# Optimization experiments

Hardware: AMD Instinct MI355X
Metric: run time of the kernel (lower is better)

Reference implementation:

```python
import jax, jax.numpy as jnp
import numpy as np

B, S, E, H = 8, 512, 1024, 16
D = E // H  # head_dim = 64


def _rope_tables(seq_len, head_dim):
    inv_freq = 1.0 / (10000.0 ** (np.arange(0, head_dim, 2, dtype=np.float32) / head_dim))
    pos = np.arange(seq_len, dtype=np.float32)
    ang = np.einsum('i,j->ij', pos, inv_freq)  # [S, D/2]
    return jnp.asarray(np.cos(ang)), jnp.asarray(np.sin(ang))


def setup_inputs() -> dict:
    key = jax.random.key(0)
    ks = jax.random.split(key, 12)
    std = 1.0 / np.sqrt(E)
    inp = {
        'x_q': jax.random.normal(ks[0], (B, S, E), jnp.float32),
        'x_k': jax.random.normal(ks[1], (B, S, E), jnp.float32),
        'x_v': jax.random.normal(ks[2], (B, S, E), jnp.float32),
        'Wq': jax.random.normal(ks[3], (E, E), jnp.float32) * std,
        'bq': jnp.zeros((E,), jnp.float32),
        'Wk': jax.random.normal(ks[4], (E, E), jnp.float32) * std,
        'bk': jnp.zeros((E,), jnp.float32),
        'Wv': jax.random.normal(ks[5], (E, E), jnp.float32) * std,
        'bv': jnp.zeros((E,), jnp.float32),
        'Wo': jax.random.normal(ks[6], (E, E), jnp.float32) * std,
        'bo': jnp.zeros((E,), jnp.float32),
        'temperature': jnp.ones((), jnp.float32),
    }
    cos, sin = _rope_tables(S, D)
    inp['cos'] = cos
    inp['sin'] = sin
    return inp


def reference(x_q, x_k, x_v, Wq, bq, Wk, bk, Wv, bv, Wo, bo, temperature, cos, sin):
    b, s, e = x_q.shape
    h, d = H, D

    def proj(x, W, bias):
        # torch Linear: x @ W.T + b ; then split heads -> [b, h, s, d]
        y = jnp.einsum('bse,fe->bsf', x, W) + bias
        return y.reshape(b, s, h, d).transpose(0, 2, 1, 3)

    q = proj(x_q, Wq, bq)
    k = proj(x_k, Wk, bk)
    v = proj(x_v, Wv, bv)

    c = cos[:s]  # [s, d/2]
    sn = sin[:s]

    def rope(t):
        # interleaved pairing: view as [..., d/2, 2]
        t2 = t.reshape(b, h, s, d // 2, 2)
        t0, t1 = t2[..., 0], t2[..., 1]
        r = jnp.stack([t0 * c - t1 * sn, t0 * sn + t1 * c], axis=-1)
        return r.reshape(b, h, s, d)

    q = rope(q)
    k = rope(k)

    def l2norm(t):
        # torch F.normalize: x / max(||x||, eps)
        n = jnp.sqrt(jnp.sum(t * t, axis=-1, keepdims=True))
        return t / jnp.maximum(n, 1e-12)

    q = l2norm(q)
    k = l2norm(k)

    scores = jnp.einsum('bhqd,bhkd->bhqk', q, k) * temperature
    attn = jax.nn.softmax(scores, axis=-1)
    out = jnp.einsum('bhqk,bhkd->bhqd', attn, v)
    out = out.transpose(0, 2, 1, 3).reshape(b, s, e)
    return jnp.einsum('bse,fe->bsf', out, Wo) + bo
```

## Files before the change

### kernel.cpp

```cpp
#include <hip/hip_runtime.h>
#include <stdint.h>

#define DEV __device__ __forceinline__

typedef __bf16 bf16x8 __attribute__((ext_vector_type(8)));
typedef float f32x4 __attribute__((ext_vector_type(4)));
typedef unsigned short u16;
typedef u16 u16x8 __attribute__((ext_vector_type(8)));
typedef u16 u16x4 __attribute__((ext_vector_type(4)));
typedef __attribute__((address_space(3))) uint8_t lds8;
typedef __attribute__((address_space(1))) const uint8_t glb8;

constexpr int Bb = 8, Ss = 512, Ee = 1024, Hh = 16;
constexpr int BS = Bb * Ss;

DEV u16 f2bf(float f) {
  union { float f; uint32_t u; } v; v.f = f;
  return (u16)((v.u + 0x7FFFu + ((v.u >> 16) & 1u)) >> 16);
}
DEV bf16x8 ldsbf8(const u16* p) {
  u16x8 u = *(const u16x8*)p;
  return __builtin_bit_cast(bf16x8, u);
}
DEV f32x4 mfma16(bf16x8 a, bf16x8 b, f32x4 c) {
  return __builtin_amdgcn_mfma_f32_16x16x32_bf16(a, b, c, 0, 0, 0);
}

struct ConvArgs {
  const float* s[7];
  u16* d[7];
  int n[7];
};

__global__ __launch_bounds__(256) void convert_k(ConvArgs a) {
  int z = blockIdx.y;
  int base = (blockIdx.x * 256 + threadIdx.x) * 8;
  if (base >= a.n[z]) return;
  const float4* sp = (const float4*)(a.s[z] + base);
  float4 v0 = sp[0], v1 = sp[1];
  u16x8 o;
  o[0] = f2bf(v0.x); o[1] = f2bf(v0.y); o[2] = f2bf(v0.z); o[3] = f2bf(v0.w);
  o[4] = f2bf(v1.x); o[5] = f2bf(v1.y); o[6] = f2bf(v1.z); o[7] = f2bf(v1.w);
  *(u16x8*)(a.d[z] + base) = o;
}

DEV void gemm_main(const u16* __restrict__ A, const u16* __restrict__ W,
                   f32x4 (&acc)[4][4]) {
  constexpr int K = Ee;
  __shared__ u16 sA[128 * 64], sB[128 * 64];
  const int tid = threadIdx.x, lane = tid & 63, wid = tid >> 6;
  const int lr = lane & 15, lh = lane >> 4;
  const int m0 = blockIdx.x * 128, n0 = blockIdx.y * 128;
  const int wm = (wid >> 1) * 64, wn = (wid & 1) * 64;
#pragma unroll
  for (int a = 0; a < 4; ++a)
#pragma unroll
    for (int q = 0; q < 4; ++q) acc[a][q] = f32x4{0.f, 0.f, 0.f, 0.f};

  for (int k0 = 0; k0 < K; k0 += 64) {
    __syncthreads();
#pragma unroll
    for (int j = 0; j < 4; ++j) {
      int c0 = wid * 256 + j * 64;
      int c = c0 + lane;
      int r = c >> 3, p = (c & 7) ^ (r & 7);
      const u16* ga = A + (size_t)(m0 + r) * K + k0 + p * 8;
      const u16* gb = W + (size_t)(n0 + r) * K + k0 + p * 8;
      __builtin_amdgcn_global_load_lds((glb8*)ga, (lds8*)&sA[c0 * 8], 16, 0, 0);
      __builtin_amdgcn_global_load_lds((glb8*)gb, (lds8*)&sB[c0 * 8], 16, 0, 0);
    }
    __syncthreads();
#pragma unroll
    for (int ks = 0; ks < 2; ++ks) {
      bf16x8 af[4], bfv[4];
#pragma unroll
      for (int t = 0; t < 4; ++t) {
        af[t] = ldsbf8(&sA[(wm + t * 16 + lr) * 64 + ((ks * 4 + lh) ^ (lr & 7)) * 8]);
        bfv[t] = ldsbf8(&sB[(wn + t * 16 + lr) * 64 + ((ks * 4 + lh) ^ (lr & 7)) * 8]);
      }
#pragma unroll
      for (int mt = 0; mt < 4; ++mt)
#pragma unroll
        for (int nt = 0; nt < 4; ++nt)
          acc[mt][nt] = mfma16(af[mt], bfv[nt], acc[mt][nt]);
    }
  }
}

__global__ __launch_bounds__(256) void gemm_qkv(
    const u16* xq, const u16* xk, const u16* xv,
    const u16* wq, const u16* wk, const u16* wv,
    const float* bq_, const float* bk_, const float* bv_,
    const float* __restrict__ cosT, const float* __restrict__ sinT,
    u16* qh, u16* kh, u16* vt) {
  int z = blockIdx.z;
  const u16* A = z == 0 ? xq : (z == 1 ? xk : xv);
  const u16* W = z == 0 ? wq : (z == 1 ? wk : wv);
  const float* bias = z == 0 ? bq_ : (z == 1 ? bk_ : bv_);
  f32x4 acc[4][4];
  gemm_main(A, W, acc);

  const int tid = threadIdx.x, lane = tid & 63, wid = tid >> 6;
  const int lr = lane & 15, lh = lane >> 4;
  const int m0 = blockIdx.x * 128, n0 = blockIdx.y * 128;
  const int wm = (wid >> 1) * 64, wn = (wid & 1) * 64;
  const int hh = (n0 + wn) >> 6;
  const int b = m0 >> 9;
  const int sbase = (m0 & 511) + wm;
  float bv[4];
#pragma unroll
  for (int nt = 0; nt < 4; ++nt) bv[nt] = bias[n0 + wn + nt * 16 + lr];

  if (z < 2) {
    u16* dst = z ? kh : qh;
#pragma unroll
    for (int mt = 0; mt < 4; ++mt) {
#pragma unroll
      for (int i = 0; i < 4; ++i) {
        int s = sbase + mt * 16 + lh * 4 + i;
        float r[4];
        float ss = 0.f;
#pragma unroll
        for (int nt = 0; nt < 4; ++nt) {
          float t = acc[mt][nt][i] + bv[nt];
          float pr = __shfl_xor(t, 1);
          int ii = (nt * 16 + lr) >> 1;
          float c = cosT[s * 32 + ii], sn = sinT[s * 32 + ii];
          r[nt] = (lane & 1) ? (pr * sn + t * c) : (t * c - pr * sn);
          ss += r[nt] * r[nt];
        }
#pragma unroll
        for (int m = 1; m < 16; m <<= 1) ss += __shfl_xor(ss, m);
        float inv = 1.f / fmaxf(sqrtf(ss), 1e-12f);
        size_t ob = ((size_t)(b * Hh + hh) * Ss + s) * 64;
#pragma unroll
        for (int nt = 0; nt < 4; ++nt) dst[ob + nt * 16 + lr] = f2bf(r[nt] * inv);
      }
    }
  } else {
#pragma unroll
    for (int mt = 0; mt < 4; ++mt) {
#pragma unroll
      for (int nt = 0; nt < 4; ++nt) {
        int d = nt * 16 + lr;
        int s4 = sbase + mt * 16 + lh * 4;
        u16x4 pv;
#pragma unroll
        for (int i = 0; i < 4; ++i) pv[i] = f2bf(acc[mt][nt][i] + bv[nt]);
        *(u16x4*)(vt + ((size_t)(b * Hh + hh) * 64 + d) * Ss + s4) = pv;
      }
    }
  }
}

__global__ __launch_bounds__(256) void gemm_fin(
    const u16* __restrict__ ctx, const u16* __restrict__ wo,
    const float* __restrict__ bo_, float* __restrict__ out) {
  f32x4 acc[4][4];
  gemm_main(ctx, wo, acc);
  const int tid = threadIdx.x, lane = tid & 63, wid = tid >> 6;
  const int lr = lane & 15, lh = lane >> 4;
  const int m0 = blockIdx.x * 128, n0 = blockIdx.y * 128;
  const int wm = (wid >> 1) * 64, wn = (wid & 1) * 64;
#pragma unroll
  for (int nt = 0; nt < 4; ++nt) {
    int col = n0 + wn + nt * 16 + lr;
    float bvv = bo_[col];
#pragma unroll
    for (int mt = 0; mt < 4; ++mt)
#pragma unroll
      for (int i = 0; i < 4; ++i) {
        int row = m0 + wm + mt * 16 + lh * 4 + i;
        out[(size_t)row * Ee + col] = acc[mt][nt][i] + bvv;
      }
  }
}

__global__ __launch_bounds__(256) void attn_k(
    const u16* __restrict__ qh, const u16* __restrict__ kh, const u16* __restrict__ vT,
    const float* __restrict__ temp, u16* __restrict__ ctx) {
  __shared__ u16 sQ[64 * 64], sK[64 * 64], sV[64 * 64];
  __shared__ u16 sP[4][16 * 64];
  int tid = threadIdx.x, lane = tid & 63, wid = tid >> 6;
  int lr = lane & 15, lh = lane >> 4;
  int qb = blockIdx.x, h = blockIdx.y, b = blockIdx.z;
  float T = temp[0];
  size_t bh = (size_t)b * Hh + h;
  const u16* Qg = qh + (bh * Ss + qb * 64) * 64;
  const u16* Kg = kh + bh * Ss * 64;
  const u16* Vg = vT + bh * 64 * Ss;

#pragma unroll
  for (int j = 0; j < 2; ++j) {
    int c = tid + j * 256;
    int r = c >> 3, p = c & 7;
    *(u16x8*)(&sQ[r * 64 + (p ^ (r & 7)) * 8]) = *(const u16x8*)(Qg + c * 8);
  }
  __syncthreads();
  bf16x8 qf[2];
  {
    int rq = wid * 16 + lr;
    qf[0] = ldsbf8(&sQ[rq * 64 + ((0 + lh) ^ (lr & 7)) * 8]);
    qf[1] = ldsbf8(&sQ[rq * 64 + ((4 + lh) ^ (lr & 7)) * 8]);
  }
  f32x4 o[4];
#pragma unroll
  for (int nt = 0; nt < 4; ++nt) o[nt] = f32x4{0.f, 0.f, 0.f, 0.f};
  float mrow[4] = {-1e30f, -1e30f, -1e30f, -1e30f};
  float lrow[4] = {0.f, 0.f, 0.f, 0.f};
  u16* sPw = sP[wid];

  for (int kb = 0; kb < Ss / 64; ++kb) {
    __syncthreads();
    const u16* Kt = Kg + (size_t)kb * 64 * 64;
#pragma unroll
    for (int j = 0; j < 2; ++j) {
      int c = tid + j * 256;
      int r = c >> 3, p = c & 7;
      int sl = (p ^ (r & 7)) * 8;
      *(u16x8*)(&sK[r * 64 + sl]) = *(const u16x8*)(Kt + c * 8);
      *(u16x8*)(&sV[r * 64 + sl]) = *(const u16x8*)(Vg + (size_t)r * Ss + kb * 64 + p * 8);
    }
    __syncthreads();
    f32x4 sc[4];
#pragma unroll
    for (int nt = 0; nt < 4; ++nt) sc[nt] = f32x4{0.f, 0.f, 0.f, 0.f};
#pragma unroll
    for (int ks = 0; ks < 2; ++ks)
#pragma unroll
      for (int nt = 0; nt < 4; ++nt) {
        int rk = nt * 16 + lr;
        bf16x8 kf = ldsbf8(&sK[rk * 64 + ((ks * 4 + lh) ^ (lr & 7)) * 8]);
        sc[nt] = mfma16(qf[ks], kf, sc[nt]);
      }
    float mb[4], mn[4], scl[4], psum[4];
#pragma unroll
    for (int nt = 0; nt < 4; ++nt)
#pragma unroll
      for (int i = 0; i < 4; ++i) sc[nt][i] *= T;
#pragma unroll
    for (int i = 0; i < 4; ++i) {
      mb[i] = fmaxf(fmaxf(sc[0][i], sc[1][i]), fmaxf(sc[2][i], sc[3][i]));
#pragma unroll
      for (int m = 1; m < 16; m <<= 1) mb[i] = fmaxf(mb[i], __shfl_xor(mb[i], m));
      mn[i] = fmaxf(mrow[i], mb[i]);
      scl[i] = __expf(mrow[i] - mn[i]);
      psum[i] = 0.f;
    }
#pragma unroll
    for (int nt = 0; nt < 4; ++nt)
#pragma unroll
      for (int i = 0; i < 4; ++i) {
        float p = __expf(sc[nt][i] - mn[i]);
        psum[i] += p;
        int kk = nt * 16 + lr;
        int rowp = lh * 4 + i;
        sPw[rowp * 64 + ((kk >> 3) ^ (rowp & 7)) * 8 + (kk & 7)] = f2bf(p);
      }
#pragma unroll
    for (int i = 0; i < 4; ++i) {
#pragma unroll
      for (int m = 1; m < 16; m <<= 1) psum[i] += __shfl_xor(psum[i], m);
      lrow[i] = lrow[i] * scl[i] + psum[i];
      mrow[i] = mn[i];
    }
#pragma unroll
    for (int nt = 0; nt < 4; ++nt)
#pragma unroll
      for (int i = 0; i < 4; ++i) o[nt][i] *= scl[i];
#pragma unroll
    for (int ks = 0; ks < 2; ++ks) {
      bf16x8 pf = ldsbf8(&sPw[lr * 64 + ((ks * 4 + lh) ^ (lr & 7)) * 8]);
#pragma unroll
      for (int nt = 0; nt < 4; ++nt) {
        int dv = nt * 16 + lr;
        bf16x8 vf = ldsbf8(&sV[dv * 64 + ((ks * 4 + lh) ^ (lr & 7)) * 8]);
        o[nt] = mfma16(pf, vf, o[nt]);
      }
    }
  }
#pragma unroll
  for (int nt = 0; nt < 4; ++nt) {
    int d = nt * 16 + lr;
#pragma unroll
    for (int i = 0; i < 4; ++i) {
      int row = qb * 64 + wid * 16 + lh * 4 + i;
      float val = o[nt][i] / lrow[i];
      ctx[((size_t)b * Ss + row) * Ee + h * 64 + d] = f2bf(val);
    }
  }
}

extern "C" void kernel_launch(void* const* d_in, const int* in_sizes, int n_in,
                              void* d_out, int out_size, void* d_ws, size_t ws_size,
                              hipStream_t stream) {
  const float* x_q = (const float*)d_in[0];
  const float* x_k = (const float*)d_in[1];
  const float* x_v = (const float*)d_in[2];
  const float* Wq = (const float*)d_in[3];
  const float* bq = (const float*)d_in[4];
  const float* Wk = (const float*)d_in[5];
  const float* bk = (const float*)d_in[6];
  const float* Wv = (const float*)d_in[7];
  const float* bv = (const float*)d_in[8];
  const float* Wo = (const float*)d_in[9];
  const float* bo = (const float*)d_in[10];
  const float* temp = (const float*)d_in[11];
  const float* cosT = (const float*)d_in[12];
  const float* sinT = (const float*)d_in[13];

  char* ws = (char*)d_ws;
  constexpr size_t MB = 1ull << 20;
  u16* XQb = (u16*)(ws + 0 * MB);
  u16* XKb = (u16*)(ws + 8 * MB);
  u16* XVb = (u16*)(ws + 16 * MB);
  u16* WOb = (u16*)(ws + 24 * MB);
  u16* QH  = (u16*)(ws + 26 * MB);
  u16* KH  = (u16*)(ws + 34 * MB);
  u16* VT  = (u16*)(ws + 42 * MB);
  u16* CTX = XKb;
  u16* WQb = (u16*)d_out;
  u16* WKb = (u16*)((char*)d_out + 2 * MB);
  u16* WVb = (u16*)((char*)d_out + 4 * MB);

  ConvArgs ca;
  ca.s[0] = x_q; ca.s[1] = x_k; ca.s[2] = x_v;
  ca.s[3] = Wq;  ca.s[4] = Wk;  ca.s[5] = Wv; ca.s[6] = Wo;
  ca.d[0] = XQb; ca.d[1] = XKb; ca.d[2] = XVb;
  ca.d[3] = WQb; ca.d[4] = WKb; ca.d[5] = WVb; ca.d[6] = WOb;
  int nx = BS * Ee, nw = Ee * Ee;
  ca.n[0] = nx; ca.n[1] = nx; ca.n[2] = nx;
  ca.n[3] = nw; ca.n[4] = nw; ca.n[5] = nw; ca.n[6] = nw;
  convert_k<<<dim3(nx / (256 * 8), 7), 256, 0, stream>>>(ca);

  gemm_qkv<<<dim3(BS / 128, Ee / 128, 3), 256, 0, stream>>>(
      XQb, XKb, XVb, WQb, WKb, WVb, bq, bk, bv, cosT, sinT, QH, KH, VT);
  attn_k<<<dim3(Ss / 64, Hh, Bb), 256, 0, stream>>>(QH, KH, VT, temp, CTX);
  gemm_fin<<<dim3(BS / 128, Ee / 128), 256, 0, stream>>>(CTX, WOb, bo, (float*)d_out);
}
```

Measured before the change: 224.6 us.

## Double-buffer GEMM and attention LDS tiles with async global-to-LDS prefetch

The GEMM main loop now uses two LDS buffers with K-step 32 and prefetches the next tile through global_load_lds while the current one is being computed. The swizzle is remapped so a 32-wide K slab packs two rows per 64-element line. The attention kernel loads Q, K and V with direct global-to-LDS copies instead of register round-trips, double-buffers K/V so the next block's load overlaps compute, and raises wave priority around the MFMA sections. This cuts one barrier per iteration and hides load latency, at the cost of more LDS use and possibly lower occupancy.

```diff
diff --git a/kernel.cpp b/kernel.cpp
--- a/kernel.cpp
+++ b/kernel.cpp
@@ -47,44 +47,67 @@
 DEV void gemm_main(const u16* __restrict__ A, const u16* __restrict__ W,
                    f32x4 (&acc)[4][4]) {
   constexpr int K = Ee;
-  __shared__ u16 sA[128 * 64], sB[128 * 64];
+  __shared__ u16 sA[2][128 * 32], sB[2][128 * 32];
   const int tid = threadIdx.x, lane = tid & 63, wid = tid >> 6;
   const int lr = lane & 15, lh = lane >> 4;
   const int m0 = blockIdx.x * 128, n0 = blockIdx.y * 128;
   const int wm = (wid >> 1) * 64, wn = (wid & 1) * 64;
+
+  const u16* aSrc[2]; const u16* bSrc[2]; int ldsOff[2];
+#pragma unroll
+  for (int j = 0; j < 2; ++j) {
+    int c0 = j * 256 + wid * 64;
+    int c = c0 + lane;
+    int q = c >> 3, sl = c & 7;
+    int rp = sl ^ (q & 7);
+    int r = q * 2 + (rp >> 2), p = rp & 3;
+    aSrc[j] = A + (size_t)(m0 + r) * K + p * 8;
+    bSrc[j] = W + (size_t)(n0 + r) * K + p * 8;
+    ldsOff[j] = c0 * 8;
+  }
+  int offA[4], offB[4];
+#pragma unroll
+  for (int t = 0; t < 4; ++t) {
+    int ra = wm + t * 16 + lr;
+    offA[t] = (ra >> 1) * 64 + ((((ra & 1) << 2) | lh) ^ ((ra >> 1) & 7)) * 8;
+    int rb = wn + t * 16 + lr;
+    offB[t] = (rb >> 1) * 64 + ((((rb & 1) << 2) | lh) ^ ((rb >> 1) & 7)) * 8;
+  }
 #pragma unroll
   for (int a = 0; a < 4; ++a)
 #pragma unroll
     for (int q = 0; q < 4; ++q) acc[a][q] = f32x4{0.f, 0.f, 0.f, 0.f};
 
-  for (int k0 = 0; k0 < K; k0 += 64) {
+#define GSTAGE(buf, k0_)                                                       \
+  {                                                                            \
+    _Pragma("unroll") for (int j = 0; j < 2; ++j) {                            \
+      __builtin_amdgcn_global_load_lds((glb8*)(aSrc[j] + (k0_)),               \
+                                       (lds8*)&sA[buf][ldsOff[j]], 16, 0, 0);  \
+      __builtin_amdgcn_global_load_lds((glb8*)(bSrc[j] + (k0_)),               \
+                                       (lds8*)&sB[buf][ldsOff[j]], 16, 0, 0);  \
+    }                                                                          \
+  }
+
+  GSTAGE(0, 0);
+  __syncthreads();
+  int cur = 0;
+  for (int k0 = 0; k0 < K; k0 += 32) {
+    if (k0 + 32 < K) GSTAGE(cur ^ 1, k0 + 32);
+    bf16x8 af[4], bfv[4];
+#pragma unroll
+    for (int t = 0; t < 4; ++t) {
+      af[t] = ldsbf8(&sA[cur][offA[t]]);
+      bfv[t] = ldsbf8(&sB[cur][offB[t]]);
+    }
+#pragma unroll
+    for (int mt = 0; mt < 4; ++mt)
+#pragma unroll
+      for (int nt = 0; nt < 4; ++nt)
+        acc[mt][nt] = mfma16(af[mt], bfv[nt], acc[mt][nt]);
     __syncthreads();
-#pragma unroll
-    for (int j = 0; j < 4; ++j) {
-      int c0 = wid * 256 + j * 64;
-      int c = c0 + lane;
-      int r = c >> 3, p = (c & 7) ^ (r & 7);
-      const u16* ga = A + (size_t)(m0 + r) * K + k0 + p * 8;
-      const u16* gb = W + (size_t)(n0 + r) * K + k0 + p * 8;
-      __builtin_amdgcn_global_load_lds((glb8*)ga, (lds8*)&sA[c0 * 8], 16, 0, 0);
-      __builtin_amdgcn_global_load_lds((glb8*)gb, (lds8*)&sB[c0 * 8], 16, 0, 0);
-    }
-    __syncthreads();
-#pragma unroll
-    for (int ks = 0; ks < 2; ++ks) {
-      bf16x8 af[4], bfv[4];
-#pragma unroll
-      for (int t = 0; t < 4; ++t) {
-        af[t] = ldsbf8(&sA[(wm + t * 16 + lr) * 64 + ((ks * 4 + lh) ^ (lr & 7)) * 8]);
-        bfv[t] = ldsbf8(&sB[(wn + t * 16 + lr) * 64 + ((ks * 4 + lh) ^ (lr & 7)) * 8]);
-      }
-#pragma unroll
-      for (int mt = 0; mt < 4; ++mt)
-#pragma unroll
-        for (int nt = 0; nt < 4; ++nt)
-          acc[mt][nt] = mfma16(af[mt], bfv[nt], acc[mt][nt]);
-    }
-  }
+    cur ^= 1;
+  }
+#undef GSTAGE
 }
 
 __global__ __launch_bounds__(256) void gemm_qkv(
@@ -179,7 +202,7 @@
 __global__ __launch_bounds__(256) void attn_k(
     const u16* __restrict__ qh, const u16* __restrict__ kh, const u16* __restrict__ vT,
     const float* __restrict__ temp, u16* __restrict__ ctx) {
-  __shared__ u16 sQ[64 * 64], sK[64 * 64], sV[64 * 64];
+  __shared__ u16 sQ[64 * 64], sK[2][64 * 64], sV[2][64 * 64];
   __shared__ u16 sP[4][16 * 64];
   int tid = threadIdx.x, lane = tid & 63, wid = tid >> 6;
   int lr = lane & 15, lh = lane >> 4;
@@ -190,13 +213,33 @@
   const u16* Kg = kh + bh * Ss * 64;
   const u16* Vg = vT + bh * 64 * Ss;
 
+  const u16* qSrc[2]; const u16* kSrc[2]; const u16* vSrc[2]; int soff[2];
 #pragma unroll
   for (int j = 0; j < 2; ++j) {
-    int c = tid + j * 256;
-    int r = c >> 3, p = c & 7;
-    *(u16x8*)(&sQ[r * 64 + (p ^ (r & 7)) * 8]) = *(const u16x8*)(Qg + c * 8);
-  }
+    int c0 = j * 256 + wid * 64;
+    int c = c0 + lane;
+    int r = c >> 3, p = (c & 7) ^ (r & 7);
+    soff[j] = c0 * 8;
+    qSrc[j] = Qg + r * 64 + p * 8;
+    kSrc[j] = Kg + r * 64 + p * 8;
+    vSrc[j] = Vg + (size_t)r * Ss + p * 8;
+  }
+#define ASTAGE(buf, kb_)                                                        \
+  {                                                                             \
+    _Pragma("unroll") for (int j = 0; j < 2; ++j) {                             \
+      __builtin_amdgcn_global_load_lds((glb8*)(kSrc[j] + (kb_) * 4096),         \
+                                       (lds8*)&sK[buf][soff[j]], 16, 0, 0);     \
+      __builtin_amdgcn_global_load_lds((glb8*)(vSrc[j] + (kb_) * 64),           \
+                                       (lds8*)&sV[buf][soff[j]], 16, 0, 0);     \
+    }                                                                           \
+  }
+
+#pragma unroll
+  for (int j = 0; j < 2; ++j)
+    __builtin_amdgcn_global_load_lds((glb8*)qSrc[j], (lds8*)&sQ[soff[j]], 16, 0, 0);
+  ASTAGE(0, 0);
   __syncthreads();
+
   bf16x8 qf[2];
   {
     int rq = wid * 16 + lr;
@@ -209,30 +252,23 @@
   float mrow[4] = {-1e30f, -1e30f, -1e30f, -1e30f};
   float lrow[4] = {0.f, 0.f, 0.f, 0.f};
   u16* sPw = sP[wid];
+  int cur = 0;
 
   for (int kb = 0; kb < Ss / 64; ++kb) {
-    __syncthreads();
-    const u16* Kt = Kg + (size_t)kb * 64 * 64;
-#pragma unroll
-    for (int j = 0; j < 2; ++j) {
-      int c = tid + j * 256;
-      int r = c >> 3, p = c & 7;
-      int sl = (p ^ (r & 7)) * 8;
-      *(u16x8*)(&sK[r * 64 + sl]) = *(const u16x8*)(Kt + c * 8);
-      *(u16x8*)(&sV[r * 64 + sl]) = *(const u16x8*)(Vg + (size_t)r * Ss + kb * 64 + p * 8);
-    }
-    __syncthreads();
+    if (kb + 1 < Ss / 64) ASTAGE(cur ^ 1, kb + 1);
     f32x4 sc[4];
 #pragma unroll
     for (int nt = 0; nt < 4; ++nt) sc[nt] = f32x4{0.f, 0.f, 0.f, 0.f};
+    __builtin_amdgcn_s_setprio(1);
 #pragma unroll
     for (int ks = 0; ks < 2; ++ks)
 #pragma unroll
       for (int nt = 0; nt < 4; ++nt) {
         int rk = nt * 16 + lr;
-        bf16x8 kf = ldsbf8(&sK[rk * 64 + ((ks * 4 + lh) ^ (lr & 7)) * 8]);
+        bf16x8 kf = ldsbf8(&sK[cur][rk * 64 + ((ks * 4 + lh) ^ (lr & 7)) * 8]);
         sc[nt] = mfma16(qf[ks], kf, sc[nt]);
       }
+    __builtin_amdgcn_s_setprio(0);
     float mb[4], mn[4], scl[4], psum[4];
 #pragma unroll
     for (int nt = 0; nt < 4; ++nt)
@@ -268,17 +304,22 @@
     for (int nt = 0; nt < 4; ++nt)
 #pragma unroll
       for (int i = 0; i < 4; ++i) o[nt][i] *= scl[i];
+    __builtin_amdgcn_s_setprio(1);
 #pragma unroll
     for (int ks = 0; ks < 2; ++ks) {
       bf16x8 pf = ldsbf8(&sPw[lr * 64 + ((ks * 4 + lh) ^ (lr & 7)) * 8]);
 #pragma unroll
       for (int nt = 0; nt < 4; ++nt) {
         int dv = nt * 16 + lr;
-        bf16x8 vf = ldsbf8(&sV[dv * 64 + ((ks * 4 + lh) ^ (lr & 7)) * 8]);
+        bf16x8 vf = ldsbf8(&sV[cur][dv * 64 + ((ks * 4 + lh) ^ (lr & 7)) * 8]);
         o[nt] = mfma16(pf, vf, o[nt]);
       }
     }
-  }
+    __builtin_amdgcn_s_setprio(0);
+    __syncthreads();
+    cur ^= 1;
+  }
+#undef ASTAGE
 #pragma unroll
   for (int nt = 0; nt < 4; ++nt) {
     int d = nt * 16 + lr;
```

Measured after the change: 220.5 us. No clear change (-1.8%).
